# Kernel optimization log

Measured on AMD Instinct MI355X. Metric: run time of the kernel, lower is better.

## Reference

```python
import jax, jax.numpy as jnp
import numpy as np


def setup_inputs() -> dict:
    key = jax.random.key(0)
    k1, k2, k3, k4 = jax.random.split(key, 4)
    N, K, F, E = 50000, 32, 128, 16
    nodes = jax.random.normal(k1, (N, F), dtype=jnp.float32)
    nlist = jax.random.randint(k2, (N, K), 0, N, dtype=jnp.int64)
    edges = jax.random.uniform(k3, (N, K, E), dtype=jnp.float32)
    w = jax.random.normal(k4, (F, F, E), dtype=jnp.float32) * 0.05
    return {"nodes": nodes, "nlist": nlist, "edges": edges, "w": w}


def reference(nodes, nlist, edges, w):
    # gather neighbor features: [N, K, F]
    sliced = nodes[nlist]
    K = nlist.shape[1]
    # fused 3-way contraction + mean over neighbors (axis j):
    # original: einsum('ijn,ijl,lmn->ijm', edges, sliced, w).mean(axis=1)
    out = jnp.einsum('ijn,ijl,lmn->im', edges, sliced, w) / K
    return out
```

## Files before the change

### kernel.cpp

```cpp
#include <hip/hip_runtime.h>


typedef _Float16 half8  __attribute__((ext_vector_type(8)));
typedef _Float16 half4v __attribute__((ext_vector_type(4)));
typedef float    float4v __attribute__((ext_vector_type(4)));
typedef int      int4v  __attribute__((ext_vector_type(4)));
typedef unsigned int uint;

#define NF 128
#define NK 32
#define NE 16
#define RPB 32

__global__ __launch_bounds__(256) void k_prep_nodes(const float* __restrict__ src,
                                                    _Float16* __restrict__ dst, int n4) {
    int i = blockIdx.x * 256 + threadIdx.x;
    if (i < n4) {
        float4v v = ((const float4v*)src)[i];
        half4v h;
        h[0] = (_Float16)v[0]; h[1] = (_Float16)v[1];
        h[2] = (_Float16)v[2]; h[3] = (_Float16)v[3];
        ((half4v*)dst)[i] = h;
    }
}

__global__ __launch_bounds__(256) void k_prep_w(const float* __restrict__ w,
                                                _Float16* __restrict__ w2t) {
    int o  = blockIdx.x * 256 + threadIdx.x;
    int m  = o >> 11;
    int cf = o & 2047;
    int ch = cf >> 9;
    int cp = cf & 511;
    int ltq = cp >> 6;
    int n   = (cp >> 2) & 15;
    int g   = cp & 3;
    int l = ch * 32 + (ltq >> 2) * 16 + (ltq & 3) * 4 + g;
    w2t[o] = (_Float16)w[(l * NF + m) * NE + n];
}

__global__ __launch_bounds__(256, 4) void k_mp(const _Float16* __restrict__ nodes_h,
                                               const int* __restrict__ nlist,
                                               const float* __restrict__ edges,
                                               const _Float16* __restrict__ w2t,
                                               float* __restrict__ out, int N) {
    __shared__ __align__(16) _Float16 s_T[RPB * 512];
    __shared__ __align__(16) _Float16 s_G[4 * NK * 32];

    const int tid  = threadIdx.x;
    const int wv   = tid >> 6;
    const int ln   = tid & 63;
    const int quad = ln >> 4;
    const int c16  = ln & 15;
    const int row0 = blockIdx.x * RPB;

    _Float16* __restrict__ gbuf = &s_G[wv * (NK * 32)];
    const float4v zf = {0.f, 0.f, 0.f, 0.f};

    half8 fe[8];
    #pragma unroll
    for (int r = 0; r < 8; ++r) {
        int rg = row0 + wv * 8 + r; if (rg > N - 1) rg = N - 1;
        const float* ep = edges + (size_t)rg * (NK * NE) + quad * (8 * NE) + c16;
        #pragma unroll
        for (int jj = 0; jj < 8; ++jj) fe[r][jj] = (_Float16)ep[jj * NE];
    }

    const int jlane = ln >> 2;
    const int sub   = ln & 3;
    int nb0[8], nb1[8];
    #pragma unroll
    for (int r = 0; r < 8; ++r) {
        int rg = row0 + wv * 8 + r; if (rg > N - 1) rg = N - 1;
        nb0[r] = nlist[rg * NK + jlane]      << 8;
        nb1[r] = nlist[rg * NK + 16 + jlane] << 8;
    }
    const int wblk0 = (sub ^ ((jlane >> 3) & 3)) << 3;
    const int wblk1 = (sub ^ (((jlane + 16) >> 3) & 3)) << 3;

    float4v a00 = zf, a01 = zf, a10 = zf, a11 = zf;
    const char* nbase = (const char*)nodes_h;

    half8 pA0 = *(const half8*)(nbase + nb0[0] + sub * 16);
    half8 pA1 = *(const half8*)(nbase + nb1[0] + sub * 16);
    half8 pB0 = *(const half8*)(nbase + nb0[1] + sub * 16);
    half8 pB1 = *(const half8*)(nbase + nb1[1] + sub * 16);

    for (int ch = 0; ch < 4; ++ch) {
        #pragma unroll
        for (int r = 0; r < 8; ++r) {
            const int il = wv * 8 + r;
            if ((r & 1) == 0) {
                *(half8*)&gbuf[jlane * 32 + wblk0]        = pA0;
                *(half8*)&gbuf[(jlane + 16) * 32 + wblk1] = pA1;
                if (r < 6) {
                    pA0 = *(const half8*)(nbase + nb0[r + 2] + ch * 64 + sub * 16);
                    pA1 = *(const half8*)(nbase + nb1[r + 2] + ch * 64 + sub * 16);
                }
            } else {
                *(half8*)&gbuf[jlane * 32 + wblk0]        = pB0;
                *(half8*)&gbuf[(jlane + 16) * 32 + wblk1] = pB1;
                if (r < 6) {
                    pB0 = *(const half8*)(nbase + nb0[r + 2] + ch * 64 + sub * 16);
                    pB1 = *(const half8*)(nbase + nb1[r + 2] + ch * 64 + sub * 16);
                }
            }
            #pragma unroll
            for (int lt = 0; lt < 2; ++lt) {
                const int col   = lt * 16 + c16;
                const int rbase = quad * (8 * 32) + (col ^ (quad << 3));
                uint t0 = *(const unsigned short*)&gbuf[rbase + 0 * 32];
                uint t1 = *(const unsigned short*)&gbuf[rbase + 1 * 32];
                uint t2 = *(const unsigned short*)&gbuf[rbase + 2 * 32];
                uint t3 = *(const unsigned short*)&gbuf[rbase + 3 * 32];
                uint t4 = *(const unsigned short*)&gbuf[rbase + 4 * 32];
                uint t5 = *(const unsigned short*)&gbuf[rbase + 5 * 32];
                uint t6 = *(const unsigned short*)&gbuf[rbase + 6 * 32];
                uint t7 = *(const unsigned short*)&gbuf[rbase + 7 * 32];
                int4v pv;
                pv[0] = (int)(t0 | (t1 << 16));
                pv[1] = (int)(t2 | (t3 << 16));
                pv[2] = (int)(t4 | (t5 << 16));
                pv[3] = (int)(t6 | (t7 << 16));
                half8 av = __builtin_bit_cast(half8, pv);
                float4v d = __builtin_amdgcn_mfma_f32_16x16x32_f16(av, fe[r], zf, 0, 0, 0);
                const int ltq  = lt * 4 + quad;
                const int cb   = ltq * 64 + c16 * 4;
                const int phys = cb ^ ((((ltq ^ il) & 7)) << 3);
                half4v hv;
                hv[0] = (_Float16)d[0]; hv[1] = (_Float16)d[1];
                hv[2] = (_Float16)d[2]; hv[3] = (_Float16)d[3];
                *(half4v*)&s_T[il * 512 + phys] = hv;
            }
        }
        __syncthreads();

        if (ch < 3) {
            pA0 = *(const half8*)(nbase + nb0[0] + (ch + 1) * 64 + sub * 16);
            pA1 = *(const half8*)(nbase + nb1[0] + (ch + 1) * 64 + sub * 16);
            pB0 = *(const half8*)(nbase + nb0[1] + (ch + 1) * 64 + sub * 16);
            pB1 = *(const half8*)(nbase + nb1[1] + (ch + 1) * 64 + sub * 16);
        }

        const _Float16* wr0 = w2t + ((size_t)(wv * 2 + 0) * 16 + c16) * 2048 + ch * 512;
        const _Float16* wr1 = w2t + ((size_t)(wv * 2 + 1) * 16 + c16) * 2048 + ch * 512;
        #pragma unroll 4
        for (int kt = 0; kt < 16; ++kt) {
            const int cb2  = kt * 32 + quad * 8;
            const int mask = (((cb2 >> 6) ^ c16) & 7) << 3;
            half8 t0 = *(const half8*)&s_T[c16 * 512        + (cb2 ^ mask)];
            half8 t1 = *(const half8*)&s_T[(16 + c16) * 512 + (cb2 ^ mask)];
            half8 b0 = *(const half8*)(wr0 + cb2);
            half8 b1 = *(const half8*)(wr1 + cb2);
            a00 = __builtin_amdgcn_mfma_f32_16x16x32_f16(t0, b0, a00, 0, 0, 0);
            a10 = __builtin_amdgcn_mfma_f32_16x16x32_f16(t1, b0, a10, 0, 0, 0);
            a01 = __builtin_amdgcn_mfma_f32_16x16x32_f16(t0, b1, a01, 0, 0, 0);
            a11 = __builtin_amdgcn_mfma_f32_16x16x32_f16(t1, b1, a11, 0, 0, 0);
        }
        __syncthreads();
    }

    float* sf = (float*)s_T;
    const float sc = 1.0f / (float)NK;
    const int mb = (wv << 5) + c16;
    #pragma unroll
    for (int g = 0; g < 4; ++g) {
        const int r0 = quad * 4 + g;
        sf[r0 * NF + mb]             = a00[g] * sc;
        sf[r0 * NF + mb + 16]        = a01[g] * sc;
        sf[(r0 + 16) * NF + mb]      = a10[g] * sc;
        sf[(r0 + 16) * NF + mb + 16] = a11[g] * sc;
    }
    __syncthreads();
    const int lim = (N - row0) * NF;
    float* ob = out + (size_t)row0 * NF;
    #pragma unroll
    for (int u = 0; u < 4; ++u) {
        const int idx = (tid + u * 256) * 4;
        if (idx < lim) *(float4v*)&ob[idx] = *(const float4v*)&sf[idx];
    }
}

extern "C" void kernel_launch(void* const* d_in, const int* in_sizes, int n_in,
                              void* d_out, int out_size, void* d_ws, size_t ws_size,
                              hipStream_t stream) {
    const float* nodes = (const float*)d_in[0];
    const int*   nlist = (const int*)d_in[1];
    const float* edges = (const float*)d_in[2];
    const float* w     = (const float*)d_in[3];
    float* out = (float*)d_out;

    const int N = in_sizes[0] / NF;

    _Float16* w2t     = (_Float16*)d_ws;
    _Float16* nodes_h = (_Float16*)((char*)d_ws + 524288);

    const int n4 = (N * NF) / 4;
    k_prep_nodes<<<(n4 + 255) / 256, 256, 0, stream>>>(nodes, nodes_h, n4);
    k_prep_w<<<(NF * NF * NE) / 256, 256, 0, stream>>>(w, w2t);

    const int blocks = (N + RPB - 1) / RPB;
    k_mp<<<blocks, 256, 0, stream>>>(nodes_h, nlist, edges, w2t, out, N);
}
```

Measured before the change: 326.4 us.

## Gather 64 features per neighbor per pass and stash second-chunk MFMA results in registers

The neighbor-feature gather now loads 128-byte pieces (64 halves) per neighbor row in two passes instead of 64-byte pieces in four. Each pass computes the edge-contraction MFMAs for two feature chunks. The first chunk is written to shared memory immediately, and the second is held in registers (hC1) and written during the following odd chunk iteration. The aim is fewer, wider scattered global loads per neighbor and fewer gather rounds. The cost is doubled gather LDS, more live registers, and launch bounds relaxed from 4 to 3 waves per SIMD, which lowers occupancy.

```diff
diff --git a/kernel.cpp b/kernel.cpp
--- a/kernel.cpp
+++ b/kernel.cpp
@@ -38,13 +38,13 @@
     w2t[o] = (_Float16)w[(l * NF + m) * NE + n];
 }
 
-__global__ __launch_bounds__(256, 4) void k_mp(const _Float16* __restrict__ nodes_h,
+__global__ __launch_bounds__(256, 3) void k_mp(const _Float16* __restrict__ nodes_h,
                                                const int* __restrict__ nlist,
                                                const float* __restrict__ edges,
                                                const _Float16* __restrict__ w2t,
                                                float* __restrict__ out, int N) {
     __shared__ __align__(16) _Float16 s_T[RPB * 512];
-    __shared__ __align__(16) _Float16 s_G[4 * NK * 32];
+    __shared__ __align__(16) _Float16 s_G[4 * NK * 64];
 
     const int tid  = threadIdx.x;
     const int wv   = tid >> 6;
@@ -53,7 +53,7 @@
     const int c16  = ln & 15;
     const int row0 = blockIdx.x * RPB;
 
-    _Float16* __restrict__ gbuf = &s_G[wv * (NK * 32)];
+    _Float16* __restrict__ gbuf = &s_G[wv * (NK * 64)];
     const float4v zf = {0.f, 0.f, 0.f, 0.f};
 
     half8 fe[8];
@@ -65,80 +65,121 @@
         for (int jj = 0; jj < 8; ++jj) fe[r][jj] = (_Float16)ep[jj * NE];
     }
 
-    const int jlane = ln >> 2;
-    const int sub   = ln & 3;
-    int nb0[8], nb1[8];
+    const int jl8 = ln >> 3;
+    const int p8  = ln & 7;
+    int nb0[8], nb1[8], nb2[8], nb3[8];
     #pragma unroll
     for (int r = 0; r < 8; ++r) {
         int rg = row0 + wv * 8 + r; if (rg > N - 1) rg = N - 1;
-        nb0[r] = nlist[rg * NK + jlane]      << 8;
-        nb1[r] = nlist[rg * NK + 16 + jlane] << 8;
-    }
-    const int wblk0 = (sub ^ ((jlane >> 3) & 3)) << 3;
-    const int wblk1 = (sub ^ (((jlane + 16) >> 3) & 3)) << 3;
+        const int* np = nlist + rg * NK + jl8;
+        nb0[r] = np[0]  << 8;
+        nb1[r] = np[8]  << 8;
+        nb2[r] = np[16] << 8;
+        nb3[r] = np[24] << 8;
+    }
+    const char* nbase = (const char*)nodes_h + (p8 << 4);
+
+    const int wo0 = (0 * 8 + jl8) * 64 + ((p8 ^ 0) << 3);
+    const int wo1 = (1 * 8 + jl8) * 64 + ((p8 ^ 1) << 3);
+    const int wo2 = (2 * 8 + jl8) * 64 + ((p8 ^ 2) << 3);
+    const int wo3 = (3 * 8 + jl8) * 64 + ((p8 ^ 3) << 3);
 
     float4v a00 = zf, a01 = zf, a10 = zf, a11 = zf;
-    const char* nbase = (const char*)nodes_h;
-
-    half8 pA0 = *(const half8*)(nbase + nb0[0] + sub * 16);
-    half8 pA1 = *(const half8*)(nbase + nb1[0] + sub * 16);
-    half8 pB0 = *(const half8*)(nbase + nb0[1] + sub * 16);
-    half8 pB1 = *(const half8*)(nbase + nb1[1] + sub * 16);
+    half4v  hC1[8][2];
+
+    half8 pA0 = *(const half8*)(nbase + nb0[0]);
+    half8 pA1 = *(const half8*)(nbase + nb1[0]);
+    half8 pA2 = *(const half8*)(nbase + nb2[0]);
+    half8 pA3 = *(const half8*)(nbase + nb3[0]);
+    half8 pB0 = *(const half8*)(nbase + nb0[1]);
+    half8 pB1 = *(const half8*)(nbase + nb1[1]);
+    half8 pB2 = *(const half8*)(nbase + nb2[1]);
+    half8 pB3 = *(const half8*)(nbase + nb3[1]);
 
     for (int ch = 0; ch < 4; ++ch) {
-        #pragma unroll
-        for (int r = 0; r < 8; ++r) {
-            const int il = wv * 8 + r;
-            if ((r & 1) == 0) {
-                *(half8*)&gbuf[jlane * 32 + wblk0]        = pA0;
-                *(half8*)&gbuf[(jlane + 16) * 32 + wblk1] = pA1;
-                if (r < 6) {
-                    pA0 = *(const half8*)(nbase + nb0[r + 2] + ch * 64 + sub * 16);
-                    pA1 = *(const half8*)(nbase + nb1[r + 2] + ch * 64 + sub * 16);
+        if ((ch & 1) == 0) {
+            const int chb = (ch >> 1) << 7;
+            #pragma unroll
+            for (int r = 0; r < 8; ++r) {
+                const int il = wv * 8 + r;
+                if ((r & 1) == 0) {
+                    *(half8*)&gbuf[wo0] = pA0;  *(half8*)&gbuf[wo1] = pA1;
+                    *(half8*)&gbuf[wo2] = pA2;  *(half8*)&gbuf[wo3] = pA3;
+                    if (r < 6) {
+                        pA0 = *(const half8*)(nbase + nb0[r + 2] + chb);
+                        pA1 = *(const half8*)(nbase + nb1[r + 2] + chb);
+                        pA2 = *(const half8*)(nbase + nb2[r + 2] + chb);
+                        pA3 = *(const half8*)(nbase + nb3[r + 2] + chb);
+                    }
+                } else {
+                    *(half8*)&gbuf[wo0] = pB0;  *(half8*)&gbuf[wo1] = pB1;
+                    *(half8*)&gbuf[wo2] = pB2;  *(half8*)&gbuf[wo3] = pB3;
+                    if (r < 6) {
+                        pB0 = *(const half8*)(nbase + nb0[r + 2] + chb);
+                        pB1 = *(const half8*)(nbase + nb1[r + 2] + chb);
+                        pB2 = *(const half8*)(nbase + nb2[r + 2] + chb);
+                        pB3 = *(const half8*)(nbase + nb3[r + 2] + chb);
+                    }
                 }
-            } else {
-                *(half8*)&gbuf[jlane * 32 + wblk0]        = pB0;
-                *(half8*)&gbuf[(jlane + 16) * 32 + wblk1] = pB1;
-                if (r < 6) {
-                    pB0 = *(const half8*)(nbase + nb0[r + 2] + ch * 64 + sub * 16);
-                    pB1 = *(const half8*)(nbase + nb1[r + 2] + ch * 64 + sub * 16);
+                #pragma unroll
+                for (int c = 0; c < 2; ++c) {
+                    #pragma unroll
+                    for (int lt = 0; lt < 2; ++lt) {
+                        const int piece = c * 4 + lt * 2 + (c16 >> 3);
+                        const int rbase = quad * 512 + ((piece ^ quad) << 3) + (c16 & 7);
+                        uint t0 = *(const unsigned short*)&gbuf[rbase + 0 * 64];
+                        uint t1 = *(const unsigned short*)&gbuf[rbase + 1 * 64];
+                        uint t2 = *(const unsigned short*)&gbuf[rbase + 2 * 64];
+                        uint t3 = *(const unsigned short*)&gbuf[rbase + 3 * 64];
+                        uint t4 = *(const unsigned short*)&gbuf[rbase + 4 * 64];
+                        uint t5 = *(const unsigned short*)&gbuf[rbase + 5 * 64];
+                        uint t6 = *(const unsigned short*)&gbuf[rbase + 6 * 64];
+                        uint t7 = *(const unsigned short*)&gbuf[rbase + 7 * 64];
+                        int4v pv;
+                        pv[0] = (int)(t0 | (t1 << 16));
+                        pv[1] = (int)(t2 | (t3 << 16));
+                        pv[2] = (int)(t4 | (t5 << 16));
+                        pv[3] = (int)(t6 | (t7 << 16));
+                        half8 av = __builtin_bit_cast(half8, pv);
+                        float4v d = __builtin_amdgcn_mfma_f32_16x16x32_f16(av, fe[r], zf, 0, 0, 0);
+                        half4v hv;
+                        hv[0] = (_Float16)d[0]; hv[1] = (_Float16)d[1];
+                        hv[2] = (_Float16)d[2]; hv[3] = (_Float16)d[3];
+                        if (c == 0) {
+                            const int ltq  = lt * 4 + quad;
+                            const int cb   = ltq * 64 + c16 * 4;
+                            const int phys = cb ^ (((ltq ^ il) & 7) << 3);
+                            *(half4v*)&s_T[il * 512 + phys] = hv;
+                        } else {
+                            hC1[r][lt] = hv;
+                        }
+                    }
                 }
             }
+        } else {
             #pragma unroll
-            for (int lt = 0; lt < 2; ++lt) {
-                const int col   = lt * 16 + c16;
-                const int rbase = quad * (8 * 32) + (col ^ (quad << 3));
-                uint t0 = *(const unsigned short*)&gbuf[rbase + 0 * 32];
-                uint t1 = *(const unsigned short*)&gbuf[rbase + 1 * 32];
-                uint t2 = *(const unsigned short*)&gbuf[rbase + 2 * 32];
-                uint t3 = *(const unsigned short*)&gbuf[rbase + 3 * 32];
-                uint t4 = *(const unsigned short*)&gbuf[rbase + 4 * 32];
-                uint t5 = *(const unsigned short*)&gbuf[rbase + 5 * 32];
-                uint t6 = *(const unsigned short*)&gbuf[rbase + 6 * 32];
-                uint t7 = *(const unsigned short*)&gbuf[rbase + 7 * 32];
-                int4v pv;
-                pv[0] = (int)(t0 | (t1 << 16));
-                pv[1] = (int)(t2 | (t3 << 16));
-                pv[2] = (int)(t4 | (t5 << 16));
-                pv[3] = (int)(t6 | (t7 << 16));
-                half8 av = __builtin_bit_cast(half8, pv);
-                float4v d = __builtin_amdgcn_mfma_f32_16x16x32_f16(av, fe[r], zf, 0, 0, 0);
-                const int ltq  = lt * 4 + quad;
-                const int cb   = ltq * 64 + c16 * 4;
-                const int phys = cb ^ ((((ltq ^ il) & 7)) << 3);
-                half4v hv;
-                hv[0] = (_Float16)d[0]; hv[1] = (_Float16)d[1];
-                hv[2] = (_Float16)d[2]; hv[3] = (_Float16)d[3];
-                *(half4v*)&s_T[il * 512 + phys] = hv;
+            for (int r = 0; r < 8; ++r) {
+                const int il = wv * 8 + r;
+                #pragma unroll
+                for (int lt = 0; lt < 2; ++lt) {
+                    const int ltq  = lt * 4 + quad;
+                    const int cb   = ltq * 64 + c16 * 4;
+                    const int phys = cb ^ (((ltq ^ il) & 7) << 3);
+                    *(half4v*)&s_T[il * 512 + phys] = hC1[r][lt];
+                }
             }
         }
         __syncthreads();
 
-        if (ch < 3) {
-            pA0 = *(const half8*)(nbase + nb0[0] + (ch + 1) * 64 + sub * 16);
-            pA1 = *(const half8*)(nbase + nb1[0] + (ch + 1) * 64 + sub * 16);
-            pB0 = *(const half8*)(nbase + nb0[1] + (ch + 1) * 64 + sub * 16);
-            pB1 = *(const half8*)(nbase + nb1[1] + (ch + 1) * 64 + sub * 16);
+        if (ch == 1) {
+            pA0 = *(const half8*)(nbase + nb0[0] + 128);
+            pA1 = *(const half8*)(nbase + nb1[0] + 128);
+            pA2 = *(const half8*)(nbase + nb2[0] + 128);
+            pA3 = *(const half8*)(nbase + nb3[0] + 128);
+            pB0 = *(const half8*)(nbase + nb0[1] + 128);
+            pB1 = *(const half8*)(nbase + nb1[1] + 128);
+            pB2 = *(const half8*)(nbase + nb2[1] + 128);
+            pB3 = *(const half8*)(nbase + nb3[1] + 128);
         }
 
         const _Float16* wr0 = w2t + ((size_t)(wv * 2 + 0) * 16 + c16) * 2048 + ch * 512;
```

After: 395.8 us. 1.21x slower.
